# Optimization experiments

Measured on AMD Instinct MI355X. Metric: run time of the kernel, lower is better.

The kernel has to match this reference:

```python
import jax, jax.numpy as jnp
import numpy as np

L, B, T, C, H, FF = 2, 2, 2048, 512, 8, 1024
HS = C // H  # head size
EPS = 1.1920929e-07  # torch float32 finfo eps (nn.RMSNorm default)


def setup_inputs() -> dict:
    key = jax.random.key(0)
    ks = jax.random.split(key, 20)
    s = 0.02
    return {
        "hidden": jax.random.normal(ks[0], (B, T, C), jnp.float32),
        "target": jax.random.normal(ks[1], (B, T, C), jnp.float32),
        # self-attn per-head projections (bias=False)
        "Wq_s": jax.random.normal(ks[2], (L, H, C, HS)) * s,
        "Wk_s": jax.random.normal(ks[3], (L, H, C, HS)) * s,
        "Wv_s": jax.random.normal(ks[4], (L, H, C, HS)) * s,
        "Wo_s": jax.random.normal(ks[5], (L, C, C)) * s,
        "bo_s": jnp.zeros((L, C)),
        # cross-attn per-head projections
        "Wq_x": jax.random.normal(ks[6], (L, H, C, HS)) * s,
        "Wk_x": jax.random.normal(ks[7], (L, H, C, HS)) * s,
        "Wv_x": jax.random.normal(ks[8], (L, H, C, HS)) * s,
        "Wo_x": jax.random.normal(ks[9], (L, C, C)) * s,
        "bo_x": jnp.zeros((L, C)),
        # FFN
        "W1": jax.random.normal(ks[10], (L, C, FF)) * s,
        "b1": jnp.zeros((L, FF)),
        "W2": jax.random.normal(ks[11], (L, FF, C)) * s,
        "b2": jnp.zeros((L, C)),
        # RMSNorm gains ln1..ln4
        "g1": jnp.ones((L, C)),
        "g2": jnp.ones((L, C)),
        "g3": jnp.ones((L, C)),
        "g4": jnp.ones((L, C)),
    }


def _rms(x, g):
    return x * jax.lax.rsqrt(jnp.mean(x * x, axis=-1, keepdims=True) + EPS) * g


def _attn(q_in, kv_in, Wq, Wk, Wv, Wo, bo, causal):
    # q_in: [B,Tq,C], kv_in: [B,Tk,C]; W*: [H,C,HS]
    q = jnp.einsum('btc,hcd->bhtd', q_in, Wq)
    k = jnp.einsum('bsc,hcd->bhsd', kv_in, Wk)
    v = jnp.einsum('bsc,hcd->bhsd', kv_in, Wv)
    wei = jnp.einsum('bhtd,bhsd->bhts', q, k) * (HS ** -0.5)  # [B,H,Tq,Tk]
    if causal:
        Tq, Tk = q_in.shape[1], kv_in.shape[1]
        mask = jnp.tril(jnp.ones((Tq, Tk), bool))
        wei = jnp.where(mask, wei, -jnp.inf)
    wei = jax.nn.softmax(wei, axis=-1)
    out = jnp.einsum('bhts,bhsd->bhtd', wei, v)
    out = out.transpose(0, 2, 1, 3).reshape(q_in.shape[0], q_in.shape[1], C)
    return out @ Wo + bo


def reference(hidden, target, Wq_s, Wk_s, Wv_s, Wo_s, bo_s,
              Wq_x, Wk_x, Wv_x, Wo_x, bo_x,
              W1, b1, W2, b2, g1, g2, g3, g4):
    t = target
    for l in range(L):
        # masked self-attention with RMSNorm pre-norm + residual
        t = t + _attn(_rms(t, g1[l]), _rms(t, g1[l]), Wq_s[l], Wk_s[l], Wv_s[l],
                      Wo_s[l], bo_s[l], causal=True)
        # cross-attention: K/V from ln2(hidden), Q from ln3(t)
        t = t + _attn(_rms(t, g3[l]), _rms(hidden, g2[l]), Wq_x[l], Wk_x[l], Wv_x[l],
                      Wo_x[l], bo_x[l], causal=False)
        # GELU FFN
        h = _rms(t, g4[l])
        t = t + (jax.nn.gelu(h @ W1[l] + b1[l], approximate=False) @ W2[l] + b2[l])
    return t
```

## Files before the change

### kernel.cpp

```cpp
#include <hip/hip_runtime.h>
#include <hip/hip_bf16.h>
#include <math.h>

#define L 2
#define B 2
#define T 2048
#define C 512
#define H 8
#define FF 1024
#define HS 64
#define EPSV 1.1920929e-07f

typedef __hip_bfloat16 bf16;
typedef __attribute__((ext_vector_type(8))) short short8;
typedef __attribute__((ext_vector_type(4))) float f32x4;

__device__ __forceinline__ float b2f(bf16 x) { return __bfloat162float(x); }

__device__ __forceinline__ void gl16(const unsigned short* g, unsigned short* l) {
    __builtin_amdgcn_global_load_lds(
        (const __attribute__((address_space(1))) unsigned int*)g,
        (__attribute__((address_space(3))) unsigned int*)l, 16, 0, 0);
}

__global__ void detect_k(const unsigned short* __restrict__ g1bits, int* __restrict__ flag) {
    if (threadIdx.x == 0 && blockIdx.x == 0)
        *flag = (g1bits[0] != (unsigned short)0x3F80u) ? 1 : 0;
}

__device__ __forceinline__ float ld_in(const void* p, size_t i, int fl) {
    return fl ? ((const float*)p)[i] : b2f(((const bf16*)p)[i]);
}

#define QKVT_TOT 1572864
#define WO_TOT 524288
#define W12_TOT 1048576
#define SM_TOT 9216
#define ACT_TOT 2097152

struct TrArgs {
    const void *Wq_s, *Wk_s, *Wv_s, *Wq_x, *Wk_x, *Wv_x, *Wo_s, *Wo_x, *W1, *W2;
    bf16 *cQKVs, *cQKVx, *cWoTs, *cWoTx, *cW1T, *cW2T;
    const int* flag;
};

__global__ __launch_bounds__(256) void prep_tr_k(TrArgs a) {
    __shared__ float tile[32][33];
    int bid = blockIdx.x;
    int fl = *a.flag;
    const void* src; bf16* dst;
    size_t sbase;
    int srcLD, dstLD, r0, c0;
    if (bid < 3072) {
        int pid = bid >> 5, t = bid & 31;
        int which = pid / 48, rem = pid % 48;
        int l = rem / 24, rem2 = rem % 24;
        int p = rem2 >> 3, hh = rem2 & 7;
        src = which ? (p == 0 ? a.Wq_x : p == 1 ? a.Wk_x : a.Wv_x)
                    : (p == 0 ? a.Wq_s : p == 1 ? a.Wk_s : a.Wv_s);
        dst = (which ? a.cQKVx : a.cQKVs) + (size_t)l * 786432 + (size_t)(p * 512 + hh * 64) * 512;
        sbase = (size_t)(l * 8 + hh) * 32768;
        srcLD = 64; dstLD = 512;
        r0 = (t >> 1) * 32; c0 = (t & 1) * 32;
    } else if (bid < 4096) {
        int b2 = bid - 3072, pid = b2 >> 8, t = b2 & 255;
        int which = pid >> 1, l = pid & 1;
        src = which ? a.Wo_x : a.Wo_s;
        dst = (which ? a.cWoTx : a.cWoTs) + (size_t)l * 262144;
        sbase = (size_t)l * 262144;
        srcLD = 512; dstLD = 512;
        r0 = (t >> 4) * 32; c0 = (t & 15) * 32;
    } else if (bid < 5120) {
        int b2 = bid - 4096, l = b2 >> 9, t = b2 & 511;
        src = a.W1; dst = a.cW1T + (size_t)l * 524288; sbase = (size_t)l * 524288;
        srcLD = 1024; dstLD = 512;
        r0 = (t >> 5) * 32; c0 = (t & 31) * 32;
    } else {
        int b2 = bid - 5120, l = b2 >> 9, t = b2 & 511;
        src = a.W2; dst = a.cW2T + (size_t)l * 524288; sbase = (size_t)l * 524288;
        srcLD = 512; dstLD = 1024;
        r0 = (t >> 4) * 32; c0 = (t & 15) * 32;
    }
    int tx = threadIdx.x & 31, ty = threadIdx.x >> 5;
#pragma unroll
    for (int i = 0; i < 4; i++)
        tile[ty + i * 8][tx] = ld_in(src, sbase + (size_t)(r0 + ty + i * 8) * srcLD + c0 + tx, fl);
    __syncthreads();
#pragma unroll
    for (int i = 0; i < 4; i++)
        dst[(size_t)(c0 + ty + i * 8) * dstLD + r0 + tx] = __float2bfloat16(tile[tx][ty + i * 8]);
}

#define ACTQ 1048576
struct SmArgs {
    const void* sm[8];
    const void *hidden, *target;
    bf16* smallDst;
    float *hid, *t_buf;
    const int* flag;
};

__global__ void prep_small_k(SmArgs s) {
    int i = blockIdx.x * 256 + threadIdx.x;
    int fl = *s.flag;
    if (i < SM_TOT) {
        const int cum[9] = {0, 1024, 2048, 4096, 5120, 6144, 7168, 8192, 9216};
        int k = 0;
        while (i >= cum[k + 1]) k++;
        s.smallDst[i] = __float2bfloat16(ld_in(s.sm[k], i - cum[k], fl));
        return;
    }
    int q = i - SM_TOT;
    if (q >= ACTQ) return;
    int half = q >= (ACTQ / 2);
    size_t e = (size_t)(q - half * (ACTQ / 2)) * 4;
    const void* src = half ? s.target : s.hidden;
    float* dstf = half ? s.t_buf : s.hid;
    if (fl) {
        *(float4*)(dstf + e) = *(const float4*)((const float*)src + e);
    } else {
        ushort4 u = *(const ushort4*)((const unsigned short*)src + e);
        float4 v;
        v.x = __uint_as_float((unsigned)u.x << 16);
        v.y = __uint_as_float((unsigned)u.y << 16);
        v.z = __uint_as_float((unsigned)u.z << 16);
        v.w = __uint_as_float((unsigned)u.w << 16);
        *(float4*)(dstf + e) = v;
    }
}

__global__ void rmsnorm_k(const float* __restrict__ x, const bf16* __restrict__ g,
                          bf16* __restrict__ y) {
    int row = blockIdx.x;
    int tid = threadIdx.x;
    const float* xr = x + (size_t)row * C;
    float v0 = xr[tid], v1 = xr[tid + 256];
    float s = v0 * v0 + v1 * v1;
#pragma unroll
    for (int mk = 1; mk < 64; mk <<= 1) s += __shfl_xor(s, mk, 64);
    __shared__ float ws[4];
    if ((tid & 63) == 0) ws[tid >> 6] = s;
    __syncthreads();
    float sc = rsqrtf((ws[0] + ws[1] + ws[2] + ws[3]) / (float)C + EPSV);
    y[(size_t)row * C + tid] = __float2bfloat16(v0 * sc * b2f(g[tid]));
    y[(size_t)row * C + tid + 256] = __float2bfloat16(v1 * sc * b2f(g[tid + 256]));
}

__global__ void rmsnorm2_k(const float* __restrict__ xa, const bf16* __restrict__ ga,
                           bf16* __restrict__ ya, const float* __restrict__ xb,
                           const bf16* __restrict__ gb, bf16* __restrict__ yb) {
    int sel = blockIdx.y;
    const float* x = sel ? xb : xa;
    const bf16* g = sel ? gb : ga;
    bf16* y = sel ? yb : ya;
    int row = blockIdx.x;
    int tid = threadIdx.x;
    const float* xr = x + (size_t)row * C;
    float v0 = xr[tid], v1 = xr[tid + 256];
    float s = v0 * v0 + v1 * v1;
#pragma unroll
    for (int mk = 1; mk < 64; mk <<= 1) s += __shfl_xor(s, mk, 64);
    __shared__ float ws[4];
    if ((tid & 63) == 0) ws[tid >> 6] = s;
    __syncthreads();
    float sc = rsqrtf((ws[0] + ws[1] + ws[2] + ws[3]) / (float)C + EPSV);
    y[(size_t)row * C + tid] = __float2bfloat16(v0 * sc * b2f(g[tid]));
    y[(size_t)row * C + tid + 256] = __float2bfloat16(v1 * sc * b2f(g[tid + 256]));
}

struct GDesc {
    const bf16* A; const bf16* Bt; const bf16* bias; float* resid; bf16* out;
    int N, K, ldOut, ep, nblkx, blkofs, ldAB, kofs;
};
struct GBatch { GDesc d[3]; int nd; const int* flagp; };

__global__ __launch_bounds__(256) void gemm64_k(GBatch gb) {
    int bid = blockIdx.x;
    int di = 0;
    if (gb.nd > 1 && bid >= gb.d[1].blkofs) di = 1;
    if (gb.nd > 2 && bid >= gb.d[2].blkofs) di = 2;
    GDesc g = gb.d[di];
    int lb = bid - g.blkofs;
    int bx = lb % g.nblkx, by = lb / g.nblkx;
    int m0 = by * 64, n0 = bx * 64;

    __shared__ alignas(16) unsigned short As[2][64 * 64];
    __shared__ alignas(16) unsigned short Bs[2][64 * 64];
    int tid = threadIdx.x, lane = tid & 63, wave = tid >> 6;
    int wr = wave >> 1, wc = wave & 1, quad = lane >> 4, l15 = lane & 15;
    const unsigned short* Au = (const unsigned short*)g.A;
    const unsigned short* Bu = (const unsigned short*)g.Bt;

    int r0 = tid >> 3, sg = tid & 7;
    int gs = sg ^ (r0 & 7);
    const unsigned short* agp0 = Au + (size_t)(m0 + r0) * g.ldAB + g.kofs + gs * 8;
    const unsigned short* agp1 = Au + (size_t)(m0 + r0 + 32) * g.ldAB + g.kofs + gs * 8;
    const unsigned short* bgp0 = Bu + (size_t)(n0 + r0) * g.ldAB + g.kofs + gs * 8;
    const unsigned short* bgp1 = Bu + (size_t)(n0 + r0 + 32) * g.ldAB + g.kofs + gs * 8;
    int wofs = wave * 512;

    f32x4 zf = {0.f, 0.f, 0.f, 0.f};
    f32x4 acc[2][2];
    acc[0][0] = zf; acc[0][1] = zf; acc[1][0] = zf; acc[1][1] = zf;

    int sws0 = ((quad) ^ (l15 & 7)) * 8;
    int sws1 = ((4 + quad) ^ (l15 & 7)) * 8;
    int arow = wr * 32 + l15, brow = wc * 32 + l15;

    int nk = g.K >> 6;
    {
        gl16(agp0, &As[0][wofs]);
        gl16(agp1, &As[0][wofs + 2048]);
        gl16(bgp0, &Bs[0][wofs]);
        gl16(bgp1, &Bs[0][wofs + 2048]);
    }
    int buf = 0;
    for (int kt = 0; kt < nk; kt++) {
        __builtin_amdgcn_sched_barrier(0);
        __builtin_amdgcn_s_barrier();
        __builtin_amdgcn_sched_barrier(0);
        if (kt + 1 < nk) {
            int ko = (kt + 1) << 6;
            gl16(agp0 + ko, &As[buf ^ 1][wofs]);
            gl16(agp1 + ko, &As[buf ^ 1][wofs + 2048]);
            gl16(bgp0 + ko, &Bs[buf ^ 1][wofs]);
            gl16(bgp1 + ko, &Bs[buf ^ 1][wofs + 2048]);
            asm volatile("s_waitcnt vmcnt(4)" ::: "memory");
        } else {
            asm volatile("s_waitcnt vmcnt(0)" ::: "memory");
        }
        __builtin_amdgcn_sched_barrier(0);
        __builtin_amdgcn_s_barrier();
        __builtin_amdgcn_sched_barrier(0);

        const unsigned short* Ab = As[buf];
        const unsigned short* Bb = Bs[buf];
        short8 a0[2], b0[2], a1[2], b1[2];
#pragma unroll
        for (int i = 0; i < 2; i++) {
            int ra = (arow + i * 16) << 6, rb = (brow + i * 16) << 6;
            a0[i] = *(const short8*)(Ab + ra + sws0);
            a1[i] = *(const short8*)(Ab + ra + sws1);
            b0[i] = *(const short8*)(Bb + rb + sws0);
            b1[i] = *(const short8*)(Bb + rb + sws1);
        }
#pragma unroll
        for (int mi = 0; mi < 2; mi++)
#pragma unroll
            for (int ni = 0; ni < 2; ni++) {
                acc[mi][ni] =
                    __builtin_amdgcn_mfma_f32_16x16x32_bf16(a0[mi], b0[ni], acc[mi][ni], 0, 0, 0);
                acc[mi][ni] =
                    __builtin_amdgcn_mfma_f32_16x16x32_bf16(a1[mi], b1[ni], acc[mi][ni], 0, 0, 0);
            }
        buf ^= 1;
    }

    int fl4 = (g.ep == 4) ? *gb.flagp : 0;
#pragma unroll
    for (int mi = 0; mi < 2; mi++) {
#pragma unroll
        for (int ni = 0; ni < 2; ni++) {
            int colg = n0 + wc * 32 + ni * 16 + l15;
            float bv = (g.ep == 1 || g.ep == 2 || g.ep == 4) ? b2f(g.bias[colg]) : 0.f;
#pragma unroll
            for (int r2 = 0; r2 < 4; r2++) {
                int rowg = m0 + wr * 32 + mi * 16 + quad * 4 + r2;
                float v = acc[mi][ni][r2];
                size_t oi = (size_t)rowg * g.ldOut + colg;
                if (g.ep == 0) {
                    g.out[oi] = __float2bfloat16(v);
                } else if (g.ep == 1) {
                    g.resid[oi] += v + bv;
                } else if (g.ep == 2) {
                    float u = v + bv;
                    g.out[oi] = __float2bfloat16(0.5f * u * (1.f + erff(u * 0.70710678118654752f)));
                } else if (g.ep == 4) {
                    float u = g.resid[oi] + v + bv;
                    if (fl4) ((float*)g.out)[oi] = u;
                    else     g.out[oi] = __float2bfloat16(u);
                } else {
                    g.out[((size_t)((colg >> 11) * 512 + rowg) << 11) + (colg & 2047)] =
                        __float2bfloat16(v);
                }
            }
        }
    }
}

#define PST 72
__global__ __launch_bounds__(256) void attn_mfma_k(const bf16* __restrict__ qkv,
                                                   const bf16* __restrict__ vT,
                                                   bf16* __restrict__ attnout, int causal) {
    __shared__ alignas(16) unsigned short KsA[2][4096], VtA[2][4096];
    __shared__ unsigned short Ps[4][16 * PST];
    int qt = causal ? (gridDim.x - 1 - blockIdx.x) : blockIdx.x;
    int h = blockIdx.y, b = blockIdx.z;
    int tid = threadIdx.x, lane = tid & 63, w = tid >> 6;
    int quad = lane >> 4, l15 = lane & 15;
    const unsigned short* qk = (const unsigned short*)qkv;
    const unsigned short* vTp = (const unsigned short*)vT + ((size_t)b * 512 + h * 64) * T;
    size_t rowbase = (size_t)b * T;
    int koff = 512 + h * 64;
    unsigned short* Pw = Ps[w];
    bf16* Pwb = (bf16*)Pw;

    const unsigned short* qrow = qk + (rowbase + qt * 64 + w * 16 + l15) * 1536 + h * 64;
    short8 aq0 = *(const short8*)(qrow + quad * 8);
    short8 aq1 = *(const short8*)(qrow + 32 + quad * 8);

    int srow = lane >> 3;
    int ssp = (lane & 7) ^ (srow & 7);

    f32x4 zf = {0.f, 0.f, 0.f, 0.f};
    f32x4 oacc[4];
#pragma unroll
    for (int i = 0; i < 4; i++) oacc[i] = zf;
    float lpart[4] = {0.f, 0.f, 0.f, 0.f};

    int nT = causal ? (qt + 1) : (T / 64);

#pragma unroll
    for (int j = 0; j < 2; j++) {
        int c = w * 2 + j;
        int r = c * 8 + srow;
        gl16(qk + (rowbase + r) * 1536 + koff + ssp * 8, KsA[0] + c * 512);
        gl16(vTp + (size_t)r * T + ssp * 8, VtA[0] + c * 512);
    }
    __syncthreads();

    int buf = 0;
    for (int st = 0; st < nT; st++) {
        if (st + 1 < nT) {
#pragma unroll
            for (int j = 0; j < 2; j++) {
                int c = w * 2 + j;
                int r = c * 8 + srow;
                gl16(qk + (rowbase + (st + 1) * 64 + r) * 1536 + koff + ssp * 8,
                     KsA[buf ^ 1] + c * 512);
                gl16(vTp + (size_t)r * T + (st + 1) * 64 + ssp * 8, VtA[buf ^ 1] + c * 512);
            }
        }

        const unsigned short* Kb = KsA[buf];
        const unsigned short* Vb = VtA[buf];

        f32x4 sacc[4];
#pragma unroll
        for (int i = 0; i < 4; i++) sacc[i] = zf;
        __builtin_amdgcn_s_setprio(1);
#pragma unroll
        for (int ni = 0; ni < 4; ni++) {
            int rr = ni * 16 + l15;
            short8 bk0 = *(const short8*)(Kb + rr * 64 + ((quad ^ (rr & 7)) * 8));
            short8 bk1 = *(const short8*)(Kb + rr * 64 + (((4 + quad) ^ (rr & 7)) * 8));
            sacc[ni] = __builtin_amdgcn_mfma_f32_16x16x32_bf16(aq0, bk0, sacc[ni], 0, 0, 0);
            sacc[ni] = __builtin_amdgcn_mfma_f32_16x16x32_bf16(aq1, bk1, sacc[ni], 0, 0, 0);
        }
        __builtin_amdgcn_s_setprio(0);

        bool diag = causal && (st == qt);
        int qrl = w * 16 + quad * 4;
#pragma unroll
        for (int reg = 0; reg < 4; reg++) {
            float lp = 0.f;
#pragma unroll
            for (int ni = 0; ni < 4; ni++) {
                int s_l = ni * 16 + l15;
                float p = __expf(sacc[ni][reg] * 0.125f);
                if (diag && s_l > qrl + reg) p = 0.f;
                lp += p;
                Pwb[(quad * 4 + reg) * PST + s_l] = __float2bfloat16(p);
            }
            lpart[reg] += lp;
        }

        short8 ap0 = *(const short8*)(Pw + l15 * PST + quad * 8);
        short8 ap1 = *(const short8*)(Pw + l15 * PST + 32 + quad * 8);
        __builtin_amdgcn_s_setprio(1);
#pragma unroll
        for (int dj = 0; dj < 4; dj++) {
            int rr = dj * 16 + l15;
            short8 bv0 = *(const short8*)(Vb + rr * 64 + ((quad ^ (rr & 7)) * 8));
            short8 bv1 = *(const short8*)(Vb + rr * 64 + (((4 + quad) ^ (rr & 7)) * 8));
            oacc[dj] = __builtin_amdgcn_mfma_f32_16x16x32_bf16(ap0, bv0, oacc[dj], 0, 0, 0);
            oacc[dj] = __builtin_amdgcn_mfma_f32_16x16x32_bf16(ap1, bv1, oacc[dj], 0, 0, 0);
        }
        __builtin_amdgcn_s_setprio(0);

        __syncthreads();
        buf ^= 1;
    }

#pragma unroll
    for (int reg = 0; reg < 4; reg++) {
#pragma unroll
        for (int mk = 1; mk < 16; mk <<= 1) lpart[reg] += __shfl_xor(lpart[reg], mk, 64);
        lpart[reg] = 1.0f / lpart[reg];
    }
#pragma unroll
    for (int dj = 0; dj < 4; dj++) {
        int d = dj * 16 + l15;
#pragma unroll
        for (int reg = 0; reg < 4; reg++) {
            int q = w * 16 + quad * 4 + reg;
            attnout[(rowbase + qt * 64 + q) * C + h * HS + d] =
                __float2bfloat16(oacc[dj][reg] * lpart[reg]);
        }
    }
}

extern "C" void kernel_launch(void* const* d_in, const int* in_sizes, int n_in,
                              void* d_out, int out_size, void* d_ws, size_t ws_size,
                              hipStream_t stream) {
    const int BTC = B * T * C;
    const int BTF = B * T * FF;

    char* wsb = (char*)d_ws;
    int* flag = (int*)wsb;
    bf16* cur = (bf16*)(wsb + 256);
    bf16* cQKVs = cur;   cur += QKVT_TOT;
    bf16* cQKVx = cur;   cur += QKVT_TOT;
    bf16* cWoTs = cur;   cur += WO_TOT;
    bf16* cWoTx = cur;   cur += WO_TOT;
    bf16* cW1T = cur;    cur += W12_TOT;
    bf16* cW2T = cur;    cur += W12_TOT;
    bf16* smallBase = cur;
    bf16* cbo_s = cur;   cur += L * C;
    bf16* cbo_x = cur;   cur += L * C;
    bf16* cb1 = cur;     cur += L * FF;
    bf16* cb2 = cur;     cur += L * C;
    bf16* cg1 = cur;     cur += L * C;
    bf16* cg2 = cur;     cur += L * C;
    bf16* cg3 = cur;     cur += L * C;
    bf16* cg4 = cur;     cur += L * C;
    bf16* n1 = cur;      cur += BTC;
    bf16* n2 = cur;      cur += BTC;
    bf16* qkvbuf = cur;  cur += B * T * 3 * C;
    bf16* vTbuf = cur;   cur += BTC;
    bf16* attnout = cur; cur += BTC;
    bf16* h1buf = cur;   cur += BTF;
    size_t f32_off = (((char*)cur - wsb) + 255) & ~(size_t)255;
    float* t_buf = (float*)(wsb + f32_off);
    float* hid = t_buf + BTC;

    dim3 blk256(256);
    detect_k<<<1, 64, 0, stream>>>((const unsigned short*)d_in[16], flag);

    TrArgs ta;
    ta.Wq_s = d_in[2]; ta.Wk_s = d_in[3]; ta.Wv_s = d_in[4];
    ta.Wq_x = d_in[7]; ta.Wk_x = d_in[8]; ta.Wv_x = d_in[9];
    ta.Wo_s = d_in[5]; ta.Wo_x = d_in[10]; ta.W1 = d_in[12]; ta.W2 = d_in[14];
    ta.cQKVs = cQKVs; ta.cQKVx = cQKVx; ta.cWoTs = cWoTs; ta.cWoTx = cWoTx;
    ta.cW1T = cW1T; ta.cW2T = cW2T; ta.flag = flag;
    prep_tr_k<<<6144, blk256, 0, stream>>>(ta);

    SmArgs sa;
    sa.sm[0] = d_in[6];  sa.sm[1] = d_in[11]; sa.sm[2] = d_in[13]; sa.sm[3] = d_in[15];
    sa.sm[4] = d_in[16]; sa.sm[5] = d_in[17]; sa.sm[6] = d_in[18]; sa.sm[7] = d_in[19];
    sa.hidden = d_in[0]; sa.target = d_in[1];
    sa.smallDst = smallBase; sa.hid = hid; sa.t_buf = t_buf; sa.flag = flag;
    prep_small_k<<<(SM_TOT + ACTQ + 255) / 256, blk256, 0, stream>>>(sa);

    const int M = B * T;
    dim3 attngrid(T / 64, H, B);

    for (int l = 0; l < L; l++) {
        bf16* qkvW_s = cQKVs + (size_t)l * 3 * C * C;
        bf16* qkvW_x = cQKVx + (size_t)l * 3 * C * C;
        bf16* woT_s = cWoTs + (size_t)l * C * C;
        bf16* woT_x = cWoTx + (size_t)l * C * C;
        bf16* w1T = cW1T + (size_t)l * C * FF;
        bf16* w2T = cW2T + (size_t)l * FF * C;

        rmsnorm_k<<<M, blk256, 0, stream>>>(t_buf, cg1 + l * C, n1);
        {
            GBatch gb;
            gb.nd = 2; gb.flagp = flag;
            gb.d[0] = {n1, qkvW_s, nullptr, nullptr, qkvbuf, 1024, C, 3 * C, 0, 16, 0, C, 0};
            gb.d[1] = {qkvW_s + (size_t)1024 * C, n1, nullptr, nullptr, vTbuf,
                       M, C, 0, 3, 64, 1024, C, 0};
            gemm64_k<<<1024 + 512, blk256, 0, stream>>>(gb);
        }
        attn_mfma_k<<<attngrid, blk256, 0, stream>>>(qkvbuf, vTbuf, attnout, 1);
        {
            GBatch gb;
            gb.nd = 1; gb.flagp = flag;
            gb.d[0] = {attnout, woT_s, cbo_s + l * C, t_buf, nullptr, C, C, C, 1, 8, 0, C, 0};
            gemm64_k<<<512, blk256, 0, stream>>>(gb);
        }

        rmsnorm2_k<<<dim3(M, 2), blk256, 0, stream>>>(t_buf, cg3 + l * C, n1, hid, cg2 + l * C, n2);
        {
            GBatch gb;
            gb.nd = 3; gb.flagp = flag;
            gb.d[0] = {n1, qkvW_x, nullptr, nullptr, qkvbuf, C, C, 3 * C, 0, 8, 0, C, 0};
            gb.d[1] = {n2, qkvW_x + (size_t)512 * C, nullptr, nullptr, qkvbuf + C,
                       C, C, 3 * C, 0, 8, 512, C, 0};
            gb.d[2] = {qkvW_x + (size_t)1024 * C, n2, nullptr, nullptr, vTbuf,
                       M, C, 0, 3, 64, 1024, C, 0};
            gemm64_k<<<512 + 512 + 512, blk256, 0, stream>>>(gb);
        }
        attn_mfma_k<<<attngrid, blk256, 0, stream>>>(qkvbuf, vTbuf, attnout, 0);
        {
            GBatch gb;
            gb.nd = 1; gb.flagp = flag;
            gb.d[0] = {attnout, woT_x, cbo_x + l * C, t_buf, nullptr, C, C, C, 1, 8, 0, C, 0};
            gemm64_k<<<512, blk256, 0, stream>>>(gb);
        }

        rmsnorm_k<<<M, blk256, 0, stream>>>(t_buf, cg4 + l * C, n1);
        {
            GBatch gb;
            gb.nd = 1; gb.flagp = flag;
            gb.d[0] = {n1, w1T, cb1 + l * FF, nullptr, h1buf, FF, C, FF, 2, 16, 0, C, 0};
            gemm64_k<<<1024, blk256, 0, stream>>>(gb);
        }
        {
            GBatch gb;
            gb.nd = 1; gb.flagp = flag;
            if (l == L - 1) {
                gb.d[0] = {h1buf, w2T, cb2 + l * C, t_buf, (bf16*)d_out, C, FF, C, 4, 8, 0, FF, 0};
            } else {
                gb.d[0] = {h1buf, w2T, cb2 + l * C, t_buf, nullptr, C, FF, C, 1, 8, 0, FF, 0};
            }
            gemm64_k<<<512, blk256, 0, stream>>>(gb);
        }
    }
}
```

Baseline: 509.2 us.

## Vectorize RMSNorm, remap GEMM block order, fold softmax scale into Q projection

RMSNorm kernels now load float2 and store packed bf16 pairs with packed gain loads, which reduces the number of memory instructions. The GEMM block index is permuted across groups of 8 so that consecutive blocks are spread out, likely to balance work across XCDs or improve cache locality. The 1/sqrt(HS) scaling is moved into the Q-projection GEMM epilogue (new ep==5), which removes a multiply per score in attention. Folding the scale before the bf16 rounding of Q changes numerics slightly. The block remap could also hurt L2 reuse between neighbouring tiles.

```diff
diff --git a/kernel.cpp b/kernel.cpp
--- a/kernel.cpp
+++ b/kernel.cpp
@@ -16,6 +16,10 @@
 typedef __attribute__((ext_vector_type(4))) float f32x4;
 
 __device__ __forceinline__ float b2f(bf16 x) { return __bfloat162float(x); }
+__device__ __forceinline__ unsigned short bfbits(float f) {
+    bf16 t = __float2bfloat16(f);
+    return *(unsigned short*)&t;
+}
 
 __device__ __forceinline__ void gl16(const unsigned short* g, unsigned short* l) {
     __builtin_amdgcn_global_load_lds(
@@ -133,17 +137,20 @@
                           bf16* __restrict__ y) {
     int row = blockIdx.x;
     int tid = threadIdx.x;
-    const float* xr = x + (size_t)row * C;
-    float v0 = xr[tid], v1 = xr[tid + 256];
-    float s = v0 * v0 + v1 * v1;
+    const float2* xr = (const float2*)(x + (size_t)row * C);
+    float2 v = xr[tid];
+    float s = v.x * v.x + v.y * v.y;
 #pragma unroll
     for (int mk = 1; mk < 64; mk <<= 1) s += __shfl_xor(s, mk, 64);
     __shared__ float ws[4];
     if ((tid & 63) == 0) ws[tid >> 6] = s;
     __syncthreads();
     float sc = rsqrtf((ws[0] + ws[1] + ws[2] + ws[3]) / (float)C + EPSV);
-    y[(size_t)row * C + tid] = __float2bfloat16(v0 * sc * b2f(g[tid]));
-    y[(size_t)row * C + tid + 256] = __float2bfloat16(v1 * sc * b2f(g[tid + 256]));
+    unsigned gp = ((const unsigned*)g)[tid];
+    float g0 = __uint_as_float(gp << 16);
+    float g1 = __uint_as_float(gp & 0xffff0000u);
+    unsigned out = (unsigned)bfbits(v.x * sc * g0) | ((unsigned)bfbits(v.y * sc * g1) << 16);
+    ((unsigned*)y)[(size_t)row * 256 + tid] = out;
 }
 
 __global__ void rmsnorm2_k(const float* __restrict__ xa, const bf16* __restrict__ ga,
@@ -155,17 +162,20 @@
     bf16* y = sel ? yb : ya;
     int row = blockIdx.x;
     int tid = threadIdx.x;
-    const float* xr = x + (size_t)row * C;
-    float v0 = xr[tid], v1 = xr[tid + 256];
-    float s = v0 * v0 + v1 * v1;
+    const float2* xr = (const float2*)(x + (size_t)row * C);
+    float2 v = xr[tid];
+    float s = v.x * v.x + v.y * v.y;
 #pragma unroll
     for (int mk = 1; mk < 64; mk <<= 1) s += __shfl_xor(s, mk, 64);
     __shared__ float ws[4];
     if ((tid & 63) == 0) ws[tid >> 6] = s;
     __syncthreads();
     float sc = rsqrtf((ws[0] + ws[1] + ws[2] + ws[3]) / (float)C + EPSV);
-    y[(size_t)row * C + tid] = __float2bfloat16(v0 * sc * b2f(g[tid]));
-    y[(size_t)row * C + tid + 256] = __float2bfloat16(v1 * sc * b2f(g[tid + 256]));
+    unsigned gp = ((const unsigned*)g)[tid];
+    float g0 = __uint_as_float(gp << 16);
+    float g1 = __uint_as_float(gp & 0xffff0000u);
+    unsigned out = (unsigned)bfbits(v.x * sc * g0) | ((unsigned)bfbits(v.y * sc * g1) << 16);
+    ((unsigned*)y)[(size_t)row * 256 + tid] = out;
 }
 
 struct GDesc {
@@ -176,6 +186,10 @@
 
 __global__ __launch_bounds__(256) void gemm64_k(GBatch gb) {
     int bid = blockIdx.x;
+    {
+        int nb = gridDim.x;
+        if (!(nb & 7)) bid = (bid & 7) * (nb >> 3) + (bid >> 3);
+    }
     int di = 0;
     if (gb.nd > 1 && bid >= gb.d[1].blkofs) di = 1;
     if (gb.nd > 2 && bid >= gb.d[2].blkofs) di = 2;
@@ -279,6 +293,8 @@
                     float u = g.resid[oi] + v + bv;
                     if (fl4) ((float*)g.out)[oi] = u;
                     else     g.out[oi] = __float2bfloat16(u);
+                } else if (g.ep == 5) {
+                    g.out[oi] = __float2bfloat16(colg < 512 ? v * 0.125f : v);
                 } else {
                     g.out[((size_t)((colg >> 11) * 512 + rowg) << 11) + (colg & 2047)] =
                         __float2bfloat16(v);
@@ -367,7 +383,7 @@
 #pragma unroll
             for (int ni = 0; ni < 4; ni++) {
                 int s_l = ni * 16 + l15;
-                float p = __expf(sacc[ni][reg] * 0.125f);
+                float p = __expf(sacc[ni][reg]);
                 if (diag && s_l > qrl + reg) p = 0.f;
                 lp += p;
                 Pwb[(quad * 4 + reg) * PST + s_l] = __float2bfloat16(p);
@@ -477,7 +493,7 @@
         {
             GBatch gb;
             gb.nd = 2; gb.flagp = flag;
-            gb.d[0] = {n1, qkvW_s, nullptr, nullptr, qkvbuf, 1024, C, 3 * C, 0, 16, 0, C, 0};
+            gb.d[0] = {n1, qkvW_s, nullptr, nullptr, qkvbuf, 1024, C, 3 * C, 5, 16, 0, C, 0};
             gb.d[1] = {qkvW_s + (size_t)1024 * C, n1, nullptr, nullptr, vTbuf,
                        M, C, 0, 3, 64, 1024, C, 0};
             gemm64_k<<<1024 + 512, blk256, 0, stream>>>(gb);
@@ -494,7 +510,7 @@
         {
             GBatch gb;
             gb.nd = 3; gb.flagp = flag;
-            gb.d[0] = {n1, qkvW_x, nullptr, nullptr, qkvbuf, C, C, 3 * C, 0, 8, 0, C, 0};
+            gb.d[0] = {n1, qkvW_x, nullptr, nullptr, qkvbuf, C, C, 3 * C, 5, 8, 0, C, 0};
             gb.d[1] = {n2, qkvW_x + (size_t)512 * C, nullptr, nullptr, qkvbuf + C,
                        C, C, 3 * C, 0, 8, 512, C, 0};
             gb.d[2] = {qkvW_x + (size_t)1024 * C, n2, nullptr, nullptr, vTbuf,
```

Result: no change. 504.9 us, median of 2 (-0.8%).
